# Performance work log

Hardware: AMD Instinct MI355X
Metric: run time of the kernel (lower is better)

Reference implementation:

```python
import jax, jax.numpy as jnp
import numpy as np

B, T, C, H = 2, 64, 384, 768
LR, MOM, DECAY = 0.01, 0.9, 0.001


def pscan(gates, tokens):
    """parallel_scan_log: x[t] = gates[t]*x[t-1] + tokens[t] along axis 1.
    gates [B,S], tokens [B,S,...]."""
    extra = tokens.ndim - gates.ndim
    g = gates.reshape(gates.shape + (1,) * extra)
    g = jnp.clip(g, 1e-7, 1.0 - 1e-7)
    lc = jnp.cumsum(jnp.log(g), axis=1)              # log cumulative gates
    return jnp.exp(lc) * jnp.cumsum(tokens * jnp.exp(-lc), axis=1)


def setup_inputs():
    key = jax.random.key(0)
    ks = jax.random.split(key, 12)
    s = 0.02
    W0 = jax.random.normal(ks[0], (H, C), jnp.float32) * s
    W1 = jax.random.normal(ks[1], (C, H), jnp.float32) * s
    return {
        "x": jax.random.normal(ks[2], (B, T, C), jnp.float32),
        "Wq": jax.random.normal(ks[3], (C, C), jnp.float32) * s, "bq": jnp.zeros((C,), jnp.float32),
        "Wk": jax.random.normal(ks[4], (C, C), jnp.float32) * s, "bk": jnp.zeros((C,), jnp.float32),
        "Wv": jax.random.normal(ks[5], (C, C), jnp.float32) * s, "bv": jnp.zeros((C,), jnp.float32),
        "Wo": jax.random.normal(ks[6], (C, C), jnp.float32) * s, "bo": jnp.zeros((C,), jnp.float32),
        "init_query": jax.random.normal(ks[7], (1, 1, C), jnp.float32) * s,
        "sW0": jnp.broadcast_to(W0, (B, H, C)) + 0.0,
        "sb0": jnp.zeros((B, H), jnp.float32),
        "sW1": jnp.broadcast_to(W1, (B, C, H)) + 0.0,
        "sb1": jnp.zeros((B, C), jnp.float32),
    }


def reference(x, Wq, bq, Wk, bk, Wv, bv, Wo, bo, init_query, sW0, sb0, sW1, sb1):
    dt = x.dtype
    # ---- retrieval (causal: uses init_query since no previous segment) ----
    q = jnp.broadcast_to(init_query, (B, 1, C)) @ Wq.T + bq          # [B,1,C]
    h_pre = jnp.einsum('bqc,bhc->bqh', q, sW0) + sb0[:, None]
    h = h_pre * jax.nn.sigmoid(h_pre)                                 # SiLU
    pred = jnp.einsum('bqh,bch->bqc', h, sW1) + sb1[:, None]
    out = pred @ Wo.T + bo                                            # [B,1,C]

    # ---- test-time memory update: per-token MSE gradients ----
    k = x @ Wk.T + bk                                                 # [B,T,C]
    v = x @ Wv.T + bv
    h1_pre = jnp.einsum('btc,bhc->bth', k, sW0) + sb0[:, None]
    sig = jax.nn.sigmoid(h1_pre)
    h1 = h1_pre * sig
    p = jnp.einsum('bth,bch->btc', h1, sW1) + sb1[:, None]
    dp = p - v                                                        # d(MSE)/d(pred)
    dW1 = jnp.einsum('btc,bth->btch', dp, h1)                         # [B,T,C,H]
    db1 = dp
    dh1 = jnp.einsum('btc,bch->bth', dp, sW1)
    dh1p = dh1 * (sig * (1 + h1_pre * (1 - sig)))                     # SiLU grad
    dW0 = jnp.einsum('bth,btc->bthc', dh1p, k)                        # [B,T,H,C]
    db0 = dh1p

    # ---- momentum scan + decayed weight scan ----
    def update(W, g):
        surprise = -LR * g                                            # [B,T,...]
        m = pscan(jnp.full((B, T), MOM, dt), (1.0 - MOM) * surprise)  # EMA of surprises
        toks = jnp.concatenate([W[:, None], m], axis=1)               # seed with current weight
        gts = jnp.concatenate([jnp.ones((B, 1), dt),
                               jnp.full((B, T), 1.0 - DECAY, dt)], axis=1)
        return pscan(gts, toks)[:, -1]                                # final weight after segment

    nW0 = update(sW0, dW0)
    nb0 = update(sb0, db0)
    nW1 = update(sW1, dW1)
    nb1 = update(sb1, db1)
    return out, nW0, nb0, nW1, nb1
```

## Files before the change

### kernel.cpp

```cpp
#include <hip/hip_runtime.h>
#include <hip/hip_bf16.h>
#include <cmath>

#define BB 2
#define TT 64
#define CC 384
#define HH 768

#define O_OUT 0
#define O_NW0 768
#define O_NB0 (768 + 589824)
#define O_NW1 (O_NB0 + 1536)
#define O_NB1 (O_NW1 + 589824)

struct Coefs { float ct[TT]; float dfac; };

typedef __attribute__((ext_vector_type(8))) short bf16x8;
typedef __attribute__((ext_vector_type(4))) float f32x4;

__device__ __forceinline__ float bf2f(unsigned short u) {
    union { unsigned int i; float f; } x; x.i = ((unsigned int)u) << 16; return x.f;
}
__device__ __forceinline__ unsigned short f2bf(float f) {
    union { float f; unsigned int i; } u; u.f = f;
    unsigned int x = u.i;
    unsigned int r = (x + 0x7fffu + ((x >> 16) & 1u)) >> 16;
    return (unsigned short)r;
}
__device__ __forceinline__ f32x4 mfma16(bf16x8 a, bf16x8 b, f32x4 c) {
    return __builtin_amdgcn_mfma_f32_16x16x32_bf16(a, b, c, 0, 0, 0);
}
__device__ __forceinline__ bf16x8 ldbf8(const unsigned short* p) {
    return *(const bf16x8*)p;
}
__device__ __forceinline__ bf16x8 ldcvt8(const float* p) {
    float4 a = *(const float4*)p, b = *(const float4*)(p + 4);
    bf16x8 r;
    r[0] = (short)f2bf(a.x); r[1] = (short)f2bf(a.y); r[2] = (short)f2bf(a.z); r[3] = (short)f2bf(a.w);
    r[4] = (short)f2bf(b.x); r[5] = (short)f2bf(b.y); r[6] = (short)f2bf(b.z); r[7] = (short)f2bf(b.w);
    return r;
}

__global__ void __launch_bounds__(256) k_qkv(
        const float* __restrict__ x,
        const float* __restrict__ Wk, const float* __restrict__ bk,
        const float* __restrict__ Wv, const float* __restrict__ bv,
        const float* __restrict__ Wq, const float* __restrict__ bq,
        const float* __restrict__ iq,
        const float* __restrict__ sW0, const float* __restrict__ sW1,
        const float* __restrict__ Wo,
        unsigned short* __restrict__ kb_bf, float* __restrict__ vb,
        float* __restrict__ qb, float* __restrict__ warm_sink) {
    const int blk = blockIdx.x, j = threadIdx.x;
    if (blk >= 51) {
        int t = (blk - 51) * 256 + j;
        float acc = 0.f;
        for (int g = t; g < 184320; g += 512 * 256) {
            const float4* src; int off;
            if      (g < 73728)  { src = (const float4*)sW0; off = g; }
            else if (g < 147456) { src = (const float4*)sW1; off = g - 73728; }
            else                 { src = (const float4*)Wo;  off = g - 147456; }
            float4 v = src[off];
            acc += v.x + v.y + v.z + v.w;
        }
        if (acc != acc) warm_sink[0] = acc;
        return;
    }
    const int wid = j >> 6, L = j & 63;
    const int w = blk * 4 + wid;
    const int lrow = L & 15, kq = (L >> 4) * 8, quad = L >> 4;
    int mf, npair;
    if (w < 192) { mf = w % 8; npair = w / 8; }
    else         { mf = 8;     npair = 24 + (w - 192); }
    const float* Arow = (mf < 8) ? (x + (size_t)(mf * 16 + lrow) * CC) : iq;
    const int n0 = npair * 32 + lrow, n1 = n0 + 16;
    const float* B0 = (n0 < CC) ? (Wk + (size_t)n0 * CC)
                    : (n0 < 2 * CC) ? (Wv + (size_t)(n0 - CC) * CC)
                    : (Wq + (size_t)(n0 - 2 * CC) * CC);
    const float* B1 = (n1 < CC) ? (Wk + (size_t)n1 * CC)
                    : (n1 < 2 * CC) ? (Wv + (size_t)(n1 - CC) * CC)
                    : (Wq + (size_t)(n1 - 2 * CC) * CC);
    f32x4 acc0 = {0,0,0,0}, acc1 = {0,0,0,0};
    #pragma unroll 2
    for (int s = 0; s < CC / 32; ++s) {
        int k = s * 32 + kq;
        bf16x8 a = ldcvt8(Arow + k);
        bf16x8 b0 = ldcvt8(B0 + k), b1 = ldcvt8(B1 + k);
        acc0 = mfma16(a, b0, acc0); acc1 = mfma16(a, b1, acc1);
    }
    #pragma unroll
    for (int ni = 0; ni < 2; ++ni) {
        f32x4 acc = ni == 0 ? acc0 : acc1;
        int n = npair * 32 + ni * 16 + lrow;
        if (mf < 8) {
            #pragma unroll
            for (int r = 0; r < 4; ++r) {
                int m = mf * 16 + quad * 4 + r;
                float v = acc[r];
                if (n < CC) kb_bf[(size_t)m * CC + n] = f2bf(v + bk[n]);
                else        vb[(size_t)m * CC + (n - CC)] = v + bv[n - CC];
            }
        } else if (quad == 0) {
            qb[n - 2 * CC] = acc[0] + bq[n - 2 * CC];
        }
    }
}

__global__ void __launch_bounds__(256) k_h1(
        const unsigned short* __restrict__ kb_bf, const float* __restrict__ qb,
        const float* __restrict__ sW0, const float* __restrict__ sb0,
        unsigned short* __restrict__ h1_bf, float* __restrict__ dsil,
        float* __restrict__ hret) {
    const int blk = blockIdx.x, j = threadIdx.x;
    const int b = blk / 30;
    const int wid = j >> 6, L = j & 63;
    const int w = (blk % 30) * 4 + wid;
    const int mf = w % 5, npair = w / 5;
    const int lrow = L & 15, kq = (L >> 4) * 8, quad = L >> 4;
    const unsigned short* Abf = kb_bf + (size_t)(b * TT + mf * 16 + lrow) * CC;
    const int n0 = npair * 32 + lrow;
    const float* B0 = sW0 + (size_t)(b * HH + n0) * CC;
    const float* B1 = B0 + 16 * CC;
    f32x4 acc0 = {0,0,0,0}, acc1 = {0,0,0,0};
    if (mf < 4) {
        #pragma unroll 2
        for (int s = 0; s < CC / 32; ++s) {
            int k = s * 32 + kq;
            bf16x8 a = ldbf8(Abf + k);
            bf16x8 b0 = ldcvt8(B0 + k), b1 = ldcvt8(B1 + k);
            acc0 = mfma16(a, b0, acc0); acc1 = mfma16(a, b1, acc1);
        }
    } else {
        #pragma unroll 2
        for (int s = 0; s < CC / 32; ++s) {
            int k = s * 32 + kq;
            bf16x8 a = ldcvt8(qb + k);
            bf16x8 b0 = ldcvt8(B0 + k), b1 = ldcvt8(B1 + k);
            acc0 = mfma16(a, b0, acc0); acc1 = mfma16(a, b1, acc1);
        }
    }
    #pragma unroll
    for (int ni = 0; ni < 2; ++ni) {
        f32x4 acc = ni == 0 ? acc0 : acc1;
        int n = npair * 32 + ni * 16 + lrow;
        float bias = sb0[b * HH + n];
        if (mf < 4) {
            #pragma unroll
            for (int r = 0; r < 4; ++r) {
                int t = mf * 16 + quad * 4 + r;
                float pre = acc[r] + bias;
                float sig = 1.f / (1.f + expf(-pre));
                size_t idx = (size_t)(b * TT + t) * HH + n;
                h1_bf[idx] = f2bf(pre * sig);
                dsil[idx]  = sig * (1.f + pre * (1.f - sig));
            }
        } else if (quad == 0) {
            float pre = acc[0] + bias;
            float sig = 1.f / (1.f + expf(-pre));
            hret[b * HH + n] = pre * sig;
        }
    }
}

__global__ void __launch_bounds__(256) k_p(
        const unsigned short* __restrict__ h1_bf, const float* __restrict__ hret,
        const float* __restrict__ vb,
        const float* __restrict__ sW1, const float* __restrict__ sb1,
        unsigned short* __restrict__ dp_bf, float* __restrict__ pred) {
    const int blk = blockIdx.x, j = threadIdx.x;
    const int b = blk / 15;
    const int wid = j >> 6, L = j & 63;
    const int w = (blk % 15) * 4 + wid;
    const int mf = w % 5, npair = w / 5;
    const int lrow = L & 15, kq = (L >> 4) * 8, quad = L >> 4;
    const unsigned short* Abf = h1_bf + (size_t)(b * TT + mf * 16 + lrow) * HH;
    const float* Aq = hret + (size_t)b * HH;
    const int n0 = npair * 32 + lrow;
    const float* B0 = sW1 + (size_t)(b * CC + n0) * HH;
    const float* B1 = B0 + 16 * HH;
    f32x4 acc0 = {0,0,0,0}, acc1 = {0,0,0,0};
    if (mf < 4) {
        #pragma unroll 2
        for (int s = 0; s < HH / 32; ++s) {
            int k = s * 32 + kq;
            bf16x8 a = ldbf8(Abf + k);
            bf16x8 b0 = ldcvt8(B0 + k), b1 = ldcvt8(B1 + k);
            acc0 = mfma16(a, b0, acc0); acc1 = mfma16(a, b1, acc1);
        }
    } else {
        #pragma unroll 2
        for (int s = 0; s < HH / 32; ++s) {
            int k = s * 32 + kq;
            bf16x8 a = ldcvt8(Aq + k);
            bf16x8 b0 = ldcvt8(B0 + k), b1 = ldcvt8(B1 + k);
            acc0 = mfma16(a, b0, acc0); acc1 = mfma16(a, b1, acc1);
        }
    }
    #pragma unroll
    for (int ni = 0; ni < 2; ++ni) {
        f32x4 acc = ni == 0 ? acc0 : acc1;
        int n = npair * 32 + ni * 16 + lrow;
        float bias = sb1[b * CC + n];
        if (mf < 4) {
            #pragma unroll
            for (int r = 0; r < 4; ++r) {
                int t = mf * 16 + quad * 4 + r;
                size_t idx = (size_t)(b * TT + t) * CC + n;
                dp_bf[idx] = f2bf(acc[r] + bias - vb[idx]);
            }
        } else if (quad == 0) {
            pred[b * CC + n] = acc[0] + bias;
        }
    }
}

__global__ void __launch_bounds__(256) k_epi(
        const unsigned short* __restrict__ dp_bf,
        const unsigned short* __restrict__ h1_bf,
        const unsigned short* __restrict__ kb_bf,
        const float* __restrict__ dsil,
        const float* __restrict__ sW0, const float* __restrict__ sb0,
        const float* __restrict__ sW1, const float* __restrict__ sb1,
        const float* __restrict__ pred,
        const float* __restrict__ Wo, const float* __restrict__ bo,
        float* __restrict__ out, Coefs cf) {
    __shared__ __align__(16) unsigned char sbuf[49920];
    const int blk = blockIdx.x, j = threadIdx.x;
    if (blk < 288) {
        float* a_t = (float*)sbuf;
        float* e_t = (float*)(sbuf + 8192);
        const int b = blk / 144, rem = blk % 144;
        const int c0 = (rem / 12) * 32, h0 = (rem % 12) * 64;
        for (int i = j; i < TT * 32; i += 256) {
            int t = i >> 5, c = i & 31;
            a_t[t * 32 + c] = cf.ct[t] * bf2f(dp_bf[((size_t)(b * TT + t)) * CC + c0 + c]);
        }
        for (int i = j; i < TT * 64; i += 256) {
            int t = i >> 6, h = i & 63;
            e_t[t * 64 + h] = bf2f(h1_bf[((size_t)(b * TT + t)) * HH + h0 + h]);
        }
        __syncthreads();
        const int ci = j & 31, hb = (j >> 5) * 8;
        float acc[8] = {0, 0, 0, 0, 0, 0, 0, 0};
        for (int t = 0; t < TT; ++t) {
            float av = a_t[t * 32 + ci];
            #pragma unroll
            for (int m = 0; m < 8; ++m) acc[m] += av * e_t[t * 64 + hb + m];
        }
        const size_t idx = ((size_t)b * CC + c0 + ci) * HH + h0 + hb;
        const float4* w4 = (const float4*)(sW1 + idx);
        float4 wa = w4[0], wb = w4[1];
        float4 o0, o1;
        o0.x = cf.dfac * wa.x - acc[0]; o0.y = cf.dfac * wa.y - acc[1];
        o0.z = cf.dfac * wa.z - acc[2]; o0.w = cf.dfac * wa.w - acc[3];
        o1.x = cf.dfac * wb.x - acc[4]; o1.y = cf.dfac * wb.y - acc[5];
        o1.z = cf.dfac * wb.z - acc[6]; o1.w = cf.dfac * wb.w - acc[7];
        *(float4*)(out + O_NW1 + idx) = o0;
        *(float4*)(out + O_NW1 + idx + 4) = o1;
        if (h0 == 0 && j < 32) {
            float s = 0.f;
            for (int t = 0; t < TT; ++t) s += a_t[t * 32 + j];
            out[O_NB1 + b * CC + c0 + j] = cf.dfac * sb1[b * CC + c0 + j] - s;
        }
    } else if (blk < 576) {
        unsigned short* ldsT = (unsigned short*)sbuf;
        float* a_t = (float*)(sbuf + 25344);
        float* e_t = (float*)(sbuf + 25344 + 8192);
        const int u = blk - 288;
        const int b = u / 144, rem = u % 144;
        const int h0 = (rem / 6) * 32, c0 = (rem % 6) * 64;
        {
            const int hl = j & 31, cs = j >> 5;
            const float* base = sW1 + (size_t)b * CC * HH + h0 + hl;
            for (int c = cs; c < CC; c += 8)
                ldsT[c * 33 + hl] = f2bf(base[(size_t)c * HH]);
        }
        for (int i = j; i < TT * 64; i += 256) {
            int t = i >> 6, c = i & 63;
            e_t[t * 64 + c] = bf2f(kb_bf[((size_t)(b * TT + t)) * CC + c0 + c]);
        }
        __syncthreads();
        const int wid = j >> 6, L = j & 63;
        const int lrow = L & 15, kq = (L >> 4) * 8, quad = L >> 4;
        const unsigned short* Abf = dp_bf + (size_t)(b * TT + wid * 16 + lrow) * CC;
        f32x4 acc0 = {0,0,0,0}, acc1 = {0,0,0,0};
        for (int s = 0; s < CC / 32; ++s) {
            int k = s * 32 + kq;
            bf16x8 a = ldbf8(Abf + k);
            bf16x8 b0, b1;
            #pragma unroll
            for (int i = 0; i < 8; ++i) {
                b0[i] = (short)ldsT[(k + i) * 33 + lrow];
                b1[i] = (short)ldsT[(k + i) * 33 + 16 + lrow];
            }
            acc0 = mfma16(a, b0, acc0); acc1 = mfma16(a, b1, acc1);
        }
        #pragma unroll
        for (int ni = 0; ni < 2; ++ni) {
            f32x4 acc = ni == 0 ? acc0 : acc1;
            int hl = ni * 16 + lrow;
            #pragma unroll
            for (int r = 0; r < 4; ++r) {
                int t = wid * 16 + quad * 4 + r;
                float ds = dsil[(size_t)(b * TT + t) * HH + h0 + hl];
                a_t[t * 32 + hl] = cf.ct[t] * (acc[r] * ds);
            }
        }
        __syncthreads();
        const int hi = j & 31, cb = (j >> 5) * 8;
        float acc[8] = {0, 0, 0, 0, 0, 0, 0, 0};
        for (int t = 0; t < TT; ++t) {
            float av = a_t[t * 32 + hi];
            #pragma unroll
            for (int m = 0; m < 8; ++m) acc[m] += av * e_t[t * 64 + cb + m];
        }
        const size_t idx = ((size_t)b * HH + h0 + hi) * CC + c0 + cb;
        const float4* w4 = (const float4*)(sW0 + idx);
        float4 wa = w4[0], wb = w4[1];
        float4 o0, o1;
        o0.x = cf.dfac * wa.x - acc[0]; o0.y = cf.dfac * wa.y - acc[1];
        o0.z = cf.dfac * wa.z - acc[2]; o0.w = cf.dfac * wa.w - acc[3];
        o1.x = cf.dfac * wb.x - acc[4]; o1.y = cf.dfac * wb.y - acc[5];
        o1.z = cf.dfac * wb.z - acc[6]; o1.w = cf.dfac * wb.w - acc[7];
        *(float4*)(out + O_NW0 + idx) = o0;
        *(float4*)(out + O_NW0 + idx + 4) = o1;
        if (c0 == 0 && j < 32) {
            float s = 0.f;
            for (int t = 0; t < TT; ++t) s += a_t[t * 32 + j];
            out[O_NB0 + b * HH + h0 + j] = cf.dfac * sb0[b * HH + h0 + j] - s;
        }
    } else {
        float* vecs = (float*)sbuf;
        float* part = (float*)(sbuf + 4096);
        const int rb = blk - 576;
        const int b = rb / 24, nt = rb % 24;
        if (j < CC / 4) ((float4*)vecs)[j] = ((const float4*)(pred + b * CC))[j];
        __syncthreads();
        const int nl = j & 15, ks = j >> 4;
        const int n = nt * 16 + nl;
        const float4* wr = (const float4*)(Wo + (size_t)n * CC + ks * 24);
        float s = 0.f;
        #pragma unroll
        for (int i = 0; i < 6; ++i) {
            float4 a = wr[i];
            const float* v = vecs + ks * 24 + i * 4;
            s += a.x * v[0] + a.y * v[1] + a.z * v[2] + a.w * v[3];
        }
        part[ks * 17 + nl] = s;
        __syncthreads();
        if (j < 16) {
            int n2 = nt * 16 + j;
            float acc = bo[n2];
            #pragma unroll
            for (int kk = 0; kk < 16; ++kk) acc += part[kk * 17 + j];
            out[O_OUT + b * CC + n2] = acc;
        }
    }
}

extern "C" void kernel_launch(void* const* d_in, const int* in_sizes, int n_in,
                              void* d_out, int out_size, void* d_ws, size_t ws_size,
                              hipStream_t stream) {
    const float* x   = (const float*)d_in[0];
    const float* Wq  = (const float*)d_in[1];
    const float* bq  = (const float*)d_in[2];
    const float* Wk  = (const float*)d_in[3];
    const float* bk  = (const float*)d_in[4];
    const float* Wv  = (const float*)d_in[5];
    const float* bv  = (const float*)d_in[6];
    const float* Wo  = (const float*)d_in[7];
    const float* bo  = (const float*)d_in[8];
    const float* iq  = (const float*)d_in[9];
    const float* sW0 = (const float*)d_in[10];
    const float* sb0 = (const float*)d_in[11];
    const float* sW1 = (const float*)d_in[12];
    const float* sb1 = (const float*)d_in[13];

    float* fw = (float*)d_ws;
    float* qb   = fw;
    float* hret = qb + 384;
    float* pred = hret + 1536;
    float* vb   = pred + 768;
    float* dsil = vb + 49152;
    float* warm = dsil + 98304;
    unsigned short* us = (unsigned short*)(warm + 4);
    unsigned short* kb_bf = us;
    unsigned short* h1_bf = kb_bf + 49152;
    unsigned short* dp_bf = h1_bf + 98304;

    Coefs cf;
    const double mom = 0.9, decay = 1.0 - 0.001, lr = 0.01;
    for (int s = 0; s < TT; ++s) {
        double sum = 0.0;
        for (int t = s; t < TT; ++t) sum += pow(decay, (double)(TT - 1 - t)) * pow(mom, (double)(t - s));
        cf.ct[s] = (float)(lr * (1.0 - mom) * sum);
    }
    cf.dfac = (float)pow(decay, (double)TT);

    k_qkv<<<dim3(563), dim3(256), 0, stream>>>(x, Wk, bk, Wv, bv, Wq, bq, iq, sW0, sW1, Wo,
                                               kb_bf, vb, qb, warm);
    k_h1 <<<dim3(60),  dim3(256), 0, stream>>>(kb_bf, qb, sW0, sb0, h1_bf, dsil, hret);
    k_p  <<<dim3(30),  dim3(256), 0, stream>>>(h1_bf, hret, vb, sW1, sb1, dp_bf, pred);
    k_epi<<<dim3(624), dim3(256), 0, stream>>>(dp_bf, h1_bf, kb_bf, dsil, sW0, sb0, sW1, sb1,
                                               pred, Wo, bo, (float*)d_out, cf);
}
```

Baseline: 137.0 us.

## Fuse four kernels into one persistent kernel with grid-wide barriers

Merges the qkv, h1, p and epilogue kernels into a single persistent launch of 312 blocks. Stages are separated by atomic-counter grid barriers, and the epilogue's 624 tiles are looped over the resident blocks. The aim is to remove per-kernel launch overhead and inter-kernel gaps. In exchange it adds a memset, spin-wait barriers, and idle blocks during the small middle stages, and it depends on every block being co-resident.

```diff
diff --git a/kernel.cpp b/kernel.cpp
--- a/kernel.cpp
+++ b/kernel.cpp
@@ -12,6 +12,8 @@
 #define O_NB0 (768 + 589824)
 #define O_NW1 (O_NB0 + 1536)
 #define O_NB1 (O_NW1 + 589824)
+
+#define GRID_BLKS 312
 
 struct Coefs { float ct[TT]; float dfac; };
 
@@ -41,319 +43,320 @@
     return r;
 }
 
-__global__ void __launch_bounds__(256) k_qkv(
-        const float* __restrict__ x,
-        const float* __restrict__ Wk, const float* __restrict__ bk,
-        const float* __restrict__ Wv, const float* __restrict__ bv,
-        const float* __restrict__ Wq, const float* __restrict__ bq,
-        const float* __restrict__ iq,
-        const float* __restrict__ sW0, const float* __restrict__ sW1,
-        const float* __restrict__ Wo,
-        unsigned short* __restrict__ kb_bf, float* __restrict__ vb,
-        float* __restrict__ qb, float* __restrict__ warm_sink) {
+struct KArgs {
+    const float *x, *Wq, *bq, *Wk, *bk, *Wv, *bv, *Wo, *bo, *iq;
+    const float *sW0, *sb0, *sW1, *sb1;
+    unsigned short *kb_bf, *h1_bf, *dp_bf;
+    float *vb, *qb, *hret, *pred, *dsil, *warm;
+    unsigned *bar;
+    float *out;
+    Coefs cf;
+};
+
+__device__ __forceinline__ void gsync(unsigned* bar, int which) {
+    __syncthreads();
+    if (threadIdx.x == 0) {
+        unsigned* c = bar + which * 32;
+        __threadfence();
+        __hip_atomic_fetch_add(c, 1u, __ATOMIC_ACQ_REL, __HIP_MEMORY_SCOPE_AGENT);
+        while (__hip_atomic_load(c, __ATOMIC_ACQUIRE, __HIP_MEMORY_SCOPE_AGENT) < GRID_BLKS)
+            __builtin_amdgcn_s_sleep(2);
+    }
+    __syncthreads();
+}
+
+__global__ void __launch_bounds__(256, 2) fused(KArgs A) {
+    __shared__ __align__(16) unsigned char sbuf[49920];
     const int blk = blockIdx.x, j = threadIdx.x;
-    if (blk >= 51) {
-        int t = (blk - 51) * 256 + j;
-        float acc = 0.f;
-        for (int g = t; g < 184320; g += 512 * 256) {
-            const float4* src; int off;
-            if      (g < 73728)  { src = (const float4*)sW0; off = g; }
-            else if (g < 147456) { src = (const float4*)sW1; off = g - 73728; }
-            else                 { src = (const float4*)Wo;  off = g - 147456; }
-            float4 v = src[off];
-            acc += v.x + v.y + v.z + v.w;
-        }
-        if (acc != acc) warm_sink[0] = acc;
-        return;
-    }
-    const int wid = j >> 6, L = j & 63;
-    const int w = blk * 4 + wid;
-    const int lrow = L & 15, kq = (L >> 4) * 8, quad = L >> 4;
-    int mf, npair;
-    if (w < 192) { mf = w % 8; npair = w / 8; }
-    else         { mf = 8;     npair = 24 + (w - 192); }
-    const float* Arow = (mf < 8) ? (x + (size_t)(mf * 16 + lrow) * CC) : iq;
-    const int n0 = npair * 32 + lrow, n1 = n0 + 16;
-    const float* B0 = (n0 < CC) ? (Wk + (size_t)n0 * CC)
-                    : (n0 < 2 * CC) ? (Wv + (size_t)(n0 - CC) * CC)
-                    : (Wq + (size_t)(n0 - 2 * CC) * CC);
-    const float* B1 = (n1 < CC) ? (Wk + (size_t)n1 * CC)
-                    : (n1 < 2 * CC) ? (Wv + (size_t)(n1 - CC) * CC)
-                    : (Wq + (size_t)(n1 - 2 * CC) * CC);
-    f32x4 acc0 = {0,0,0,0}, acc1 = {0,0,0,0};
-    #pragma unroll 2
-    for (int s = 0; s < CC / 32; ++s) {
-        int k = s * 32 + kq;
-        bf16x8 a = ldcvt8(Arow + k);
-        bf16x8 b0 = ldcvt8(B0 + k), b1 = ldcvt8(B1 + k);
-        acc0 = mfma16(a, b0, acc0); acc1 = mfma16(a, b1, acc1);
-    }
-    #pragma unroll
-    for (int ni = 0; ni < 2; ++ni) {
-        f32x4 acc = ni == 0 ? acc0 : acc1;
-        int n = npair * 32 + ni * 16 + lrow;
-        if (mf < 8) {
-            #pragma unroll
-            for (int r = 0; r < 4; ++r) {
-                int m = mf * 16 + quad * 4 + r;
-                float v = acc[r];
-                if (n < CC) kb_bf[(size_t)m * CC + n] = f2bf(v + bk[n]);
-                else        vb[(size_t)m * CC + (n - CC)] = v + bv[n - CC];
-            }
-        } else if (quad == 0) {
-            qb[n - 2 * CC] = acc[0] + bq[n - 2 * CC];
-        }
-    }
-}
-
-__global__ void __launch_bounds__(256) k_h1(
-        const unsigned short* __restrict__ kb_bf, const float* __restrict__ qb,
-        const float* __restrict__ sW0, const float* __restrict__ sb0,
-        unsigned short* __restrict__ h1_bf, float* __restrict__ dsil,
-        float* __restrict__ hret) {
-    const int blk = blockIdx.x, j = threadIdx.x;
-    const int b = blk / 30;
-    const int wid = j >> 6, L = j & 63;
-    const int w = (blk % 30) * 4 + wid;
-    const int mf = w % 5, npair = w / 5;
-    const int lrow = L & 15, kq = (L >> 4) * 8, quad = L >> 4;
-    const unsigned short* Abf = kb_bf + (size_t)(b * TT + mf * 16 + lrow) * CC;
-    const int n0 = npair * 32 + lrow;
-    const float* B0 = sW0 + (size_t)(b * HH + n0) * CC;
-    const float* B1 = B0 + 16 * CC;
-    f32x4 acc0 = {0,0,0,0}, acc1 = {0,0,0,0};
-    if (mf < 4) {
+
+    if (blk < 51) {
+        const int wid = j >> 6, L = j & 63;
+        const int w = blk * 4 + wid;
+        const int lrow = L & 15, kq = (L >> 4) * 8, quad = L >> 4;
+        int mf, npair;
+        if (w < 192) { mf = w % 8; npair = w / 8; }
+        else         { mf = 8;     npair = 24 + (w - 192); }
+        const float* Arow = (mf < 8) ? (A.x + (size_t)(mf * 16 + lrow) * CC) : A.iq;
+        const int n0 = npair * 32 + lrow, n1 = n0 + 16;
+        const float* B0 = (n0 < CC) ? (A.Wk + (size_t)n0 * CC)
+                        : (n0 < 2 * CC) ? (A.Wv + (size_t)(n0 - CC) * CC)
+                        : (A.Wq + (size_t)(n0 - 2 * CC) * CC);
+        const float* B1 = (n1 < CC) ? (A.Wk + (size_t)n1 * CC)
+                        : (n1 < 2 * CC) ? (A.Wv + (size_t)(n1 - CC) * CC)
+                        : (A.Wq + (size_t)(n1 - 2 * CC) * CC);
+        f32x4 acc0 = {0,0,0,0}, acc1 = {0,0,0,0};
         #pragma unroll 2
         for (int s = 0; s < CC / 32; ++s) {
             int k = s * 32 + kq;
-            bf16x8 a = ldbf8(Abf + k);
+            bf16x8 a = ldcvt8(Arow + k);
             bf16x8 b0 = ldcvt8(B0 + k), b1 = ldcvt8(B1 + k);
-            acc0 = mfma16(a, b0, acc0); acc1 = mfma16(a, b1, acc1);
-        }
-    } else {
-        #pragma unroll 2
-        for (int s = 0; s < CC / 32; ++s) {
-            int k = s * 32 + kq;
-            bf16x8 a = ldcvt8(qb + k);
-            bf16x8 b0 = ldcvt8(B0 + k), b1 = ldcvt8(B1 + k);
-            acc0 = mfma16(a, b0, acc0); acc1 = mfma16(a, b1, acc1);
-        }
-    }
-    #pragma unroll
-    for (int ni = 0; ni < 2; ++ni) {
-        f32x4 acc = ni == 0 ? acc0 : acc1;
-        int n = npair * 32 + ni * 16 + lrow;
-        float bias = sb0[b * HH + n];
-        if (mf < 4) {
-            #pragma unroll
-            for (int r = 0; r < 4; ++r) {
-                int t = mf * 16 + quad * 4 + r;
-                float pre = acc[r] + bias;
-                float sig = 1.f / (1.f + expf(-pre));
-                size_t idx = (size_t)(b * TT + t) * HH + n;
-                h1_bf[idx] = f2bf(pre * sig);
-                dsil[idx]  = sig * (1.f + pre * (1.f - sig));
-            }
-        } else if (quad == 0) {
-            float pre = acc[0] + bias;
-            float sig = 1.f / (1.f + expf(-pre));
-            hret[b * HH + n] = pre * sig;
-        }
-    }
-}
-
-__global__ void __launch_bounds__(256) k_p(
-        const unsigned short* __restrict__ h1_bf, const float* __restrict__ hret,
-        const float* __restrict__ vb,
-        const float* __restrict__ sW1, const float* __restrict__ sb1,
-        unsigned short* __restrict__ dp_bf, float* __restrict__ pred) {
-    const int blk = blockIdx.x, j = threadIdx.x;
-    const int b = blk / 15;
-    const int wid = j >> 6, L = j & 63;
-    const int w = (blk % 15) * 4 + wid;
-    const int mf = w % 5, npair = w / 5;
-    const int lrow = L & 15, kq = (L >> 4) * 8, quad = L >> 4;
-    const unsigned short* Abf = h1_bf + (size_t)(b * TT + mf * 16 + lrow) * HH;
-    const float* Aq = hret + (size_t)b * HH;
-    const int n0 = npair * 32 + lrow;
-    const float* B0 = sW1 + (size_t)(b * CC + n0) * HH;
-    const float* B1 = B0 + 16 * HH;
-    f32x4 acc0 = {0,0,0,0}, acc1 = {0,0,0,0};
-    if (mf < 4) {
-        #pragma unroll 2
-        for (int s = 0; s < HH / 32; ++s) {
-            int k = s * 32 + kq;
-            bf16x8 a = ldbf8(Abf + k);
-            bf16x8 b0 = ldcvt8(B0 + k), b1 = ldcvt8(B1 + k);
-            acc0 = mfma16(a, b0, acc0); acc1 = mfma16(a, b1, acc1);
-        }
-    } else {
-        #pragma unroll 2
-        for (int s = 0; s < HH / 32; ++s) {
-            int k = s * 32 + kq;
-            bf16x8 a = ldcvt8(Aq + k);
-            bf16x8 b0 = ldcvt8(B0 + k), b1 = ldcvt8(B1 + k);
-            acc0 = mfma16(a, b0, acc0); acc1 = mfma16(a, b1, acc1);
-        }
-    }
-    #pragma unroll
-    for (int ni = 0; ni < 2; ++ni) {
-        f32x4 acc = ni == 0 ? acc0 : acc1;
-        int n = npair * 32 + ni * 16 + lrow;
-        float bias = sb1[b * CC + n];
-        if (mf < 4) {
-            #pragma unroll
-            for (int r = 0; r < 4; ++r) {
-                int t = mf * 16 + quad * 4 + r;
-                size_t idx = (size_t)(b * TT + t) * CC + n;
-                dp_bf[idx] = f2bf(acc[r] + bias - vb[idx]);
-            }
-        } else if (quad == 0) {
-            pred[b * CC + n] = acc[0] + bias;
-        }
-    }
-}
-
-__global__ void __launch_bounds__(256) k_epi(
-        const unsigned short* __restrict__ dp_bf,
-        const unsigned short* __restrict__ h1_bf,
-        const unsigned short* __restrict__ kb_bf,
-        const float* __restrict__ dsil,
-        const float* __restrict__ sW0, const float* __restrict__ sb0,
-        const float* __restrict__ sW1, const float* __restrict__ sb1,
-        const float* __restrict__ pred,
-        const float* __restrict__ Wo, const float* __restrict__ bo,
-        float* __restrict__ out, Coefs cf) {
-    __shared__ __align__(16) unsigned char sbuf[49920];
-    const int blk = blockIdx.x, j = threadIdx.x;
-    if (blk < 288) {
-        float* a_t = (float*)sbuf;
-        float* e_t = (float*)(sbuf + 8192);
-        const int b = blk / 144, rem = blk % 144;
-        const int c0 = (rem / 12) * 32, h0 = (rem % 12) * 64;
-        for (int i = j; i < TT * 32; i += 256) {
-            int t = i >> 5, c = i & 31;
-            a_t[t * 32 + c] = cf.ct[t] * bf2f(dp_bf[((size_t)(b * TT + t)) * CC + c0 + c]);
-        }
-        for (int i = j; i < TT * 64; i += 256) {
-            int t = i >> 6, h = i & 63;
-            e_t[t * 64 + h] = bf2f(h1_bf[((size_t)(b * TT + t)) * HH + h0 + h]);
-        }
-        __syncthreads();
-        const int ci = j & 31, hb = (j >> 5) * 8;
-        float acc[8] = {0, 0, 0, 0, 0, 0, 0, 0};
-        for (int t = 0; t < TT; ++t) {
-            float av = a_t[t * 32 + ci];
-            #pragma unroll
-            for (int m = 0; m < 8; ++m) acc[m] += av * e_t[t * 64 + hb + m];
-        }
-        const size_t idx = ((size_t)b * CC + c0 + ci) * HH + h0 + hb;
-        const float4* w4 = (const float4*)(sW1 + idx);
-        float4 wa = w4[0], wb = w4[1];
-        float4 o0, o1;
-        o0.x = cf.dfac * wa.x - acc[0]; o0.y = cf.dfac * wa.y - acc[1];
-        o0.z = cf.dfac * wa.z - acc[2]; o0.w = cf.dfac * wa.w - acc[3];
-        o1.x = cf.dfac * wb.x - acc[4]; o1.y = cf.dfac * wb.y - acc[5];
-        o1.z = cf.dfac * wb.z - acc[6]; o1.w = cf.dfac * wb.w - acc[7];
-        *(float4*)(out + O_NW1 + idx) = o0;
-        *(float4*)(out + O_NW1 + idx + 4) = o1;
-        if (h0 == 0 && j < 32) {
-            float s = 0.f;
-            for (int t = 0; t < TT; ++t) s += a_t[t * 32 + j];
-            out[O_NB1 + b * CC + c0 + j] = cf.dfac * sb1[b * CC + c0 + j] - s;
-        }
-    } else if (blk < 576) {
-        unsigned short* ldsT = (unsigned short*)sbuf;
-        float* a_t = (float*)(sbuf + 25344);
-        float* e_t = (float*)(sbuf + 25344 + 8192);
-        const int u = blk - 288;
-        const int b = u / 144, rem = u % 144;
-        const int h0 = (rem / 6) * 32, c0 = (rem % 6) * 64;
-        {
-            const int hl = j & 31, cs = j >> 5;
-            const float* base = sW1 + (size_t)b * CC * HH + h0 + hl;
-            for (int c = cs; c < CC; c += 8)
-                ldsT[c * 33 + hl] = f2bf(base[(size_t)c * HH]);
-        }
-        for (int i = j; i < TT * 64; i += 256) {
-            int t = i >> 6, c = i & 63;
-            e_t[t * 64 + c] = bf2f(kb_bf[((size_t)(b * TT + t)) * CC + c0 + c]);
-        }
-        __syncthreads();
-        const int wid = j >> 6, L = j & 63;
-        const int lrow = L & 15, kq = (L >> 4) * 8, quad = L >> 4;
-        const unsigned short* Abf = dp_bf + (size_t)(b * TT + wid * 16 + lrow) * CC;
-        f32x4 acc0 = {0,0,0,0}, acc1 = {0,0,0,0};
-        for (int s = 0; s < CC / 32; ++s) {
-            int k = s * 32 + kq;
-            bf16x8 a = ldbf8(Abf + k);
-            bf16x8 b0, b1;
-            #pragma unroll
-            for (int i = 0; i < 8; ++i) {
-                b0[i] = (short)ldsT[(k + i) * 33 + lrow];
-                b1[i] = (short)ldsT[(k + i) * 33 + 16 + lrow];
-            }
             acc0 = mfma16(a, b0, acc0); acc1 = mfma16(a, b1, acc1);
         }
         #pragma unroll
         for (int ni = 0; ni < 2; ++ni) {
             f32x4 acc = ni == 0 ? acc0 : acc1;
-            int hl = ni * 16 + lrow;
+            int n = npair * 32 + ni * 16 + lrow;
+            if (mf < 8) {
+                #pragma unroll
+                for (int r = 0; r < 4; ++r) {
+                    int m = mf * 16 + quad * 4 + r;
+                    float v = acc[r];
+                    if (n < CC) A.kb_bf[(size_t)m * CC + n] = f2bf(v + A.bk[n]);
+                    else        A.vb[(size_t)m * CC + (n - CC)] = v + A.bv[n - CC];
+                }
+            } else if (quad == 0) {
+                A.qb[n - 2 * CC] = acc[0] + A.bq[n - 2 * CC];
+            }
+        }
+    } else {
+        int t = (blk - 51) * 256 + j;
+        float acc = 0.f;
+        for (int g = t; g < 331776; g += (GRID_BLKS - 51) * 256) {
+            const float4* src; int off;
+            if      (g < 147456) { src = (const float4*)A.sW0; off = g; }
+            else if (g < 294912) { src = (const float4*)A.sW1; off = g - 147456; }
+            else                 { src = (const float4*)A.Wo;  off = g - 294912; }
+            float4 v = src[off];
+            acc += v.x + v.y + v.z + v.w;
+        }
+        if (acc != acc) A.warm[0] = acc;
+    }
+
+    gsync(A.bar, 0);
+
+    if (blk < 60) {
+        const int b = blk / 30;
+        const int wid = j >> 6, L = j & 63;
+        const int w = (blk % 30) * 4 + wid;
+        const int mf = w % 5, npair = w / 5;
+        const int lrow = L & 15, kq = (L >> 4) * 8, quad = L >> 4;
+        const unsigned short* Abf = A.kb_bf + (size_t)(b * TT + mf * 16 + lrow) * CC;
+        const int n0 = npair * 32 + lrow;
+        const float* B0 = A.sW0 + (size_t)(b * HH + n0) * CC;
+        const float* B1 = B0 + 16 * CC;
+        f32x4 acc0 = {0,0,0,0}, acc1 = {0,0,0,0};
+        if (mf < 4) {
+            #pragma unroll 2
+            for (int s = 0; s < CC / 32; ++s) {
+                int k = s * 32 + kq;
+                bf16x8 a = ldbf8(Abf + k);
+                bf16x8 b0 = ldcvt8(B0 + k), b1 = ldcvt8(B1 + k);
+                acc0 = mfma16(a, b0, acc0); acc1 = mfma16(a, b1, acc1);
+            }
+        } else {
+            #pragma unroll 2
+            for (int s = 0; s < CC / 32; ++s) {
+                int k = s * 32 + kq;
+                bf16x8 a = ldcvt8(A.qb + k);
+                bf16x8 b0 = ldcvt8(B0 + k), b1 = ldcvt8(B1 + k);
+                acc0 = mfma16(a, b0, acc0); acc1 = mfma16(a, b1, acc1);
+            }
+        }
+        #pragma unroll
+        for (int ni = 0; ni < 2; ++ni) {
+            f32x4 acc = ni == 0 ? acc0 : acc1;
+            int n = npair * 32 + ni * 16 + lrow;
+            float bias = A.sb0[b * HH + n];
+            if (mf < 4) {
+                #pragma unroll
+                for (int r = 0; r < 4; ++r) {
+                    int t = mf * 16 + quad * 4 + r;
+                    float pre = acc[r] + bias;
+                    float sig = 1.f / (1.f + expf(-pre));
+                    size_t idx = (size_t)(b * TT + t) * HH + n;
+                    A.h1_bf[idx] = f2bf(pre * sig);
+                    A.dsil[idx]  = sig * (1.f + pre * (1.f - sig));
+                }
+            } else if (quad == 0) {
+                float pre = acc[0] + bias;
+                float sig = 1.f / (1.f + expf(-pre));
+                A.hret[b * HH + n] = pre * sig;
+            }
+        }
+    }
+
+    gsync(A.bar, 1);
+
+    if (blk < 30) {
+        const int b = blk / 15;
+        const int wid = j >> 6, L = j & 63;
+        const int w = (blk % 15) * 4 + wid;
+        const int mf = w % 5, npair = w / 5;
+        const int lrow = L & 15, kq = (L >> 4) * 8, quad = L >> 4;
+        const unsigned short* Abf = A.h1_bf + (size_t)(b * TT + mf * 16 + lrow) * HH;
+        const float* Aq = A.hret + (size_t)b * HH;
+        const int n0 = npair * 32 + lrow;
+        const float* B0 = A.sW1 + (size_t)(b * CC + n0) * HH;
+        const float* B1 = B0 + 16 * HH;
+        f32x4 acc0 = {0,0,0,0}, acc1 = {0,0,0,0};
+        if (mf < 4) {
+            #pragma unroll 2
+            for (int s = 0; s < HH / 32; ++s) {
+                int k = s * 32 + kq;
+                bf16x8 a = ldbf8(Abf + k);
+                bf16x8 b0 = ldcvt8(B0 + k), b1 = ldcvt8(B1 + k);
+                acc0 = mfma16(a, b0, acc0); acc1 = mfma16(a, b1, acc1);
+            }
+        } else {
+            #pragma unroll 2
+            for (int s = 0; s < HH / 32; ++s) {
+                int k = s * 32 + kq;
+                bf16x8 a = ldcvt8(Aq + k);
+                bf16x8 b0 = ldcvt8(B0 + k), b1 = ldcvt8(B1 + k);
+                acc0 = mfma16(a, b0, acc0); acc1 = mfma16(a, b1, acc1);
+            }
+        }
+        #pragma unroll
+        for (int ni = 0; ni < 2; ++ni) {
+            f32x4 acc = ni == 0 ? acc0 : acc1;
+            int n = npair * 32 + ni * 16 + lrow;
+            float bias = A.sb1[b * CC + n];
+            if (mf < 4) {
+                #pragma unroll
+                for (int r = 0; r < 4; ++r) {
+                    int t = mf * 16 + quad * 4 + r;
+                    size_t idx = (size_t)(b * TT + t) * CC + n;
+                    A.dp_bf[idx] = f2bf(acc[r] + bias - A.vb[idx]);
+                }
+            } else if (quad == 0) {
+                A.pred[b * CC + n] = acc[0] + bias;
+            }
+        }
+    }
+
+    gsync(A.bar, 2);
+
+    for (int tile = blk; tile < 624; tile += GRID_BLKS) {
+        __syncthreads();
+        if (tile < 288) {
+            float* a_t = (float*)sbuf;
+            float* e_t = (float*)(sbuf + 8192);
+            const int b = tile / 144, rem = tile % 144;
+            const int c0 = (rem / 12) * 32, h0 = (rem % 12) * 64;
+            for (int i = j; i < TT * 32; i += 256) {
+                int t = i >> 5, c = i & 31;
+                a_t[t * 32 + c] = A.cf.ct[t] * bf2f(A.dp_bf[((size_t)(b * TT + t)) * CC + c0 + c]);
+            }
+            for (int i = j; i < TT * 64; i += 256) {
+                int t = i >> 6, h = i & 63;
+                e_t[t * 64 + h] = bf2f(A.h1_bf[((size_t)(b * TT + t)) * HH + h0 + h]);
+            }
+            __syncthreads();
+            const int ci = j & 31, hb = (j >> 5) * 8;
+            float acc[8] = {0, 0, 0, 0, 0, 0, 0, 0};
+            for (int t = 0; t < TT; ++t) {
+                float av = a_t[t * 32 + ci];
+                #pragma unroll
+                for (int m = 0; m < 8; ++m) acc[m] += av * e_t[t * 64 + hb + m];
+            }
+            const size_t idx = ((size_t)b * CC + c0 + ci) * HH + h0 + hb;
+            const float4* w4 = (const float4*)(A.sW1 + idx);
+            float4 wa = w4[0], wb = w4[1];
+            float4 o0, o1;
+            o0.x = A.cf.dfac * wa.x - acc[0]; o0.y = A.cf.dfac * wa.y - acc[1];
+            o0.z = A.cf.dfac * wa.z - acc[2]; o0.w = A.cf.dfac * wa.w - acc[3];
+            o1.x = A.cf.dfac * wb.x - acc[4]; o1.y = A.cf.dfac * wb.y - acc[5];
+            o1.z = A.cf.dfac * wb.z - acc[6]; o1.w = A.cf.dfac * wb.w - acc[7];
+            *(float4*)(A.out + O_NW1 + idx) = o0;
+            *(float4*)(A.out + O_NW1 + idx + 4) = o1;
+            if (h0 == 0 && j < 32) {
+                float s = 0.f;
+                for (int t = 0; t < TT; ++t) s += a_t[t * 32 + j];
+                A.out[O_NB1 + b * CC + c0 + j] = A.cf.dfac * A.sb1[b * CC + c0 + j] - s;
+            }
+        } else if (tile < 576) {
+            unsigned short* ldsT = (unsigned short*)sbuf;
+            float* a_t = (float*)(sbuf + 25344);
+            float* e_t = (float*)(sbuf + 25344 + 8192);
+            const int u = tile - 288;
+            const int b = u / 144, rem = u % 144;
+            const int h0 = (rem / 6) * 32, c0 = (rem % 6) * 64;
+            {
+                const int hl = j & 31, cs = j >> 5;
+                const float* base = A.sW1 + (size_t)b * CC * HH + h0 + hl;
+                for (int c = cs; c < CC; c += 8)
+                    ldsT[c * 33 + hl] = f2bf(base[(size_t)c * HH]);
+            }
+            for (int i = j; i < TT * 64; i += 256) {
+                int t = i >> 6, c = i & 63;
+                e_t[t * 64 + c] = bf2f(A.kb_bf[((size_t)(b * TT + t)) * CC + c0 + c]);
+            }
+            __syncthreads();
+            const int wid = j >> 6, L = j & 63;
+            const int lrow = L & 15, kq = (L >> 4) * 8, quad = L >> 4;
+            const unsigned short* Abf = A.dp_bf + (size_t)(b * TT + wid * 16 + lrow) * CC;
+            f32x4 acc0 = {0,0,0,0}, acc1 = {0,0,0,0};
+            for (int s = 0; s < CC / 32; ++s) {
+                int k = s * 32 + kq;
+                bf16x8 a = ldbf8(Abf + k);
+                bf16x8 b0, b1;
+                #pragma unroll
+                for (int i = 0; i < 8; ++i) {
+                    b0[i] = (short)ldsT[(k + i) * 33 + lrow];
+                    b1[i] = (short)ldsT[(k + i) * 33 + 16 + lrow];
+                }
+                acc0 = mfma16(a, b0, acc0); acc1 = mfma16(a, b1, acc1);
+            }
             #pragma unroll
-            for (int r = 0; r < 4; ++r) {
-                int t = wid * 16 + quad * 4 + r;
-                float ds = dsil[(size_t)(b * TT + t) * HH + h0 + hl];
-                a_t[t * 32 + hl] = cf.ct[t] * (acc[r] * ds);
-            }
-        }
-        __syncthreads();
-        const int hi = j & 31, cb = (j >> 5) * 8;
-        float acc[8] = {0, 0, 0, 0, 0, 0, 0, 0};
-        for (int t = 0; t < TT; ++t) {
-            float av = a_t[t * 32 + hi];
+            for (int ni = 0; ni < 2; ++ni) {
+                f32x4 acc = ni == 0 ? acc0 : acc1;
+                int hl = ni * 16 + lrow;
+                #pragma unroll
+                for (int r = 0; r < 4; ++r) {
+                    int t = wid * 16 + quad * 4 + r;
+                    float ds = A.dsil[(size_t)(b * TT + t) * HH + h0 + hl];
+                    a_t[t * 32 + hl] = A.cf.ct[t] * (acc[r] * ds);
+                }
+            }
+            __syncthreads();
+            const int hi = j & 31, cb = (j >> 5) * 8;
+            float acc[8] = {0, 0, 0, 0, 0, 0, 0, 0};
+            for (int t = 0; t < TT; ++t) {
+                float av = a_t[t * 32 + hi];
+                #pragma unroll
+                for (int m = 0; m < 8; ++m) acc[m] += av * e_t[t * 64 + cb + m];
+            }
+            const size_t idx = ((size_t)b * HH + h0 + hi) * CC + c0 + cb;
+            const float4* w4 = (const float4*)(A.sW0 + idx);
+            float4 wa = w4[0], wb = w4[1];
+            float4 o0, o1;
+            o0.x = A.cf.dfac * wa.x - acc[0]; o0.y = A.cf.dfac * wa.y - acc[1];
+            o0.z = A.cf.dfac * wa.z - acc[2]; o0.w = A.cf.dfac * wa.w - acc[3];
+            o1.x = A.cf.dfac * wb.x - acc[4]; o1.y = A.cf.dfac * wb.y - acc[5];
+            o1.z = A.cf.dfac * wb.z - acc[6]; o1.w = A.cf.dfac * wb.w - acc[7];
+            *(float4*)(A.out + O_NW0 + idx) = o0;
+            *(float4*)(A.out + O_NW0 + idx + 4) = o1;
+            if (c0 == 0 && j < 32) {
+                float s = 0.f;
+                for (int t = 0; t < TT; ++t) s += a_t[t * 32 + j];
+                A.out[O_NB0 + b * HH + h0 + j] = A.cf.dfac * A.sb0[b * HH + h0 + j] - s;
+            }
+        } else {
+            float* vecs = (float*)sbuf;
+            float* part = (float*)(sbuf + 4096);
+            const int rb = tile - 576;
+            const int b = rb / 24, nt = rb % 24;
+            if (j < CC / 4) ((float4*)vecs)[j] = ((const float4*)(A.pred + b * CC))[j];
+            __syncthreads();
+            const int nl = j & 15, ks = j >> 4;
+            const int n = nt * 16 + nl;
+            const float4* wr = (const float4*)(A.Wo + (size_t)n * CC + ks * 24);
+            float s = 0.f;
             #pragma unroll
-            for (int m = 0; m < 8; ++m) acc[m] += av * e_t[t * 64 + cb + m];
-        }
-        const size_t idx = ((size_t)b * HH + h0 + hi) * CC + c0 + cb;
-        const float4* w4 = (const float4*)(sW0 + idx);
-        float4 wa = w4[0], wb = w4[1];
-        float4 o0, o1;
-        o0.x = cf.dfac * wa.x - acc[0]; o0.y = cf.dfac * wa.y - acc[1];
-        o0.z = cf.dfac * wa.z - acc[2]; o0.w = cf.dfac * wa.w - acc[3];
-        o1.x = cf.dfac * wb.x - acc[4]; o1.y = cf.dfac * wb.y - acc[5];
-        o1.z = cf.dfac * wb.z - acc[6]; o1.w = cf.dfac * wb.w - acc[7];
-        *(float4*)(out + O_NW0 + idx) = o0;
-        *(float4*)(out + O_NW0 + idx + 4) = o1;
-        if (c0 == 0 && j < 32) {
-            float s = 0.f;
-            for (int t = 0; t < TT; ++t) s += a_t[t * 32 + j];
-            out[O_NB0 + b * HH + h0 + j] = cf.dfac * sb0[b * HH + h0 + j] - s;
-        }
-    } else {
-        float* vecs = (float*)sbuf;
-        float* part = (float*)(sbuf + 4096);
-        const int rb = blk - 576;
-        const int b = rb / 24, nt = rb % 24;
-        if (j < CC / 4) ((float4*)vecs)[j] = ((const float4*)(pred + b * CC))[j];
-        __syncthreads();
-        const int nl = j & 15, ks = j >> 4;
-        const int n = nt * 16 + nl;
-        const float4* wr = (const float4*)(Wo + (size_t)n * CC + ks * 24);
-        float s = 0.f;
-        #pragma unroll
-        for (int i = 0; i < 6; ++i) {
-            float4 a = wr[i];
-            const float* v = vecs + ks * 24 + i * 4;
-            s += a.x * v[0] + a.y * v[1] + a.z * v[2] + a.w * v[3];
-        }
-        part[ks * 17 + nl] = s;
-        __syncthreads();
-        if (j < 16) {
-            int n2 = nt * 16 + j;
-            float acc = bo[n2];
-            #pragma unroll
-            for (int kk = 0; kk < 16; ++kk) acc += part[kk * 17 + j];
-            out[O_OUT + b * CC + n2] = acc;
+            for (int i = 0; i < 6; ++i) {
+                float4 a4 = wr[i];
+                const float* v = vecs + ks * 24 + i * 4;
+                s += a4.x * v[0] + a4.y * v[1] + a4.z * v[2] + a4.w * v[3];
+            }
+            part[ks * 17 + nl] = s;
+            __syncthreads();
+            if (j < 16) {
+                int n2 = nt * 16 + j;
+                float acc = A.bo[n2];
+                #pragma unroll
+                for (int kk = 0; kk < 16; ++kk) acc += part[kk * 17 + j];
+                A.out[O_OUT + b * CC + n2] = acc;
+            }
         }
     }
 }
@@ -361,46 +364,45 @@
 extern "C" void kernel_launch(void* const* d_in, const int* in_sizes, int n_in,
                               void* d_out, int out_size, void* d_ws, size_t ws_size,
                               hipStream_t stream) {
-    const float* x   = (const float*)d_in[0];
-    const float* Wq  = (const float*)d_in[1];
-    const float* bq  = (const float*)d_in[2];
-    const float* Wk  = (const float*)d_in[3];
-    const float* bk  = (const float*)d_in[4];
-    const float* Wv  = (const float*)d_in[5];
-    const float* bv  = (const float*)d_in[6];
-    const float* Wo  = (const float*)d_in[7];
-    const float* bo  = (const float*)d_in[8];
-    const float* iq  = (const float*)d_in[9];
-    const float* sW0 = (const float*)d_in[10];
-    const float* sb0 = (const float*)d_in[11];
-    const float* sW1 = (const float*)d_in[12];
-    const float* sb1 = (const float*)d_in[13];
-
-    float* fw = (float*)d_ws;
-    float* qb   = fw;
-    float* hret = qb + 384;
-    float* pred = hret + 1536;
-    float* vb   = pred + 768;
-    float* dsil = vb + 49152;
-    float* warm = dsil + 98304;
-    unsigned short* us = (unsigned short*)(warm + 4);
-    unsigned short* kb_bf = us;
-    unsigned short* h1_bf = kb_bf + 49152;
-    unsigned short* dp_bf = h1_bf + 98304;
-
-    Coefs cf;
+    KArgs a;
+    a.x   = (const float*)d_in[0];
+    a.Wq  = (const float*)d_in[1];
+    a.bq  = (const float*)d_in[2];
+    a.Wk  = (const float*)d_in[3];
+    a.bk  = (const float*)d_in[4];
+    a.Wv  = (const float*)d_in[5];
+    a.bv  = (const float*)d_in[6];
+    a.Wo  = (const float*)d_in[7];
+    a.bo  = (const float*)d_in[8];
+    a.iq  = (const float*)d_in[9];
+    a.sW0 = (const float*)d_in[10];
+    a.sb0 = (const float*)d_in[11];
+    a.sW1 = (const float*)d_in[12];
+    a.sb1 = (const float*)d_in[13];
+
+    a.bar  = (unsigned*)d_ws;
+    float* fw = (float*)d_ws + 128;
+    a.qb   = fw;
+    a.hret = a.qb + 384;
+    a.pred = a.hret + 1536;
+    a.vb   = a.pred + 768;
+    a.dsil = a.vb + 49152;
+    a.warm = a.dsil + 98304;
+    unsigned short* us = (unsigned short*)(a.warm + 4);
+    a.kb_bf = us;
+    a.h1_bf = a.kb_bf + 49152;
+    a.dp_bf = a.h1_bf + 98304;
+
+    a.out = (float*)d_out;
+
     const double mom = 0.9, decay = 1.0 - 0.001, lr = 0.01;
     for (int s = 0; s < TT; ++s) {
         double sum = 0.0;
         for (int t = s; t < TT; ++t) sum += pow(decay, (double)(TT - 1 - t)) * pow(mom, (double)(t - s));
-        cf.ct[s] = (float)(lr * (1.0 - mom) * sum);
-    }
-    cf.dfac = (float)pow(decay, (double)TT);
-
-    k_qkv<<<dim3(563), dim3(256), 0, stream>>>(x, Wk, bk, Wv, bv, Wq, bq, iq, sW0, sW1, Wo,
-                                               kb_bf, vb, qb, warm);
-    k_h1 <<<dim3(60),  dim3(256), 0, stream>>>(kb_bf, qb, sW0, sb0, h1_bf, dsil, hret);
-    k_p  <<<dim3(30),  dim3(256), 0, stream>>>(h1_bf, hret, vb, sW1, sb1, dp_bf, pred);
-    k_epi<<<dim3(624), dim3(256), 0, stream>>>(dp_bf, h1_bf, kb_bf, dsil, sW0, sb0, sW1, sb1,
-                                               pred, Wo, bo, (float*)d_out, cf);
-}
+        a.cf.ct[s] = (float)(lr * (1.0 - mom) * sum);
+    }
+    a.cf.dfac = (float)pow(decay, (double)TT);
+
+    hipMemsetAsync(a.bar, 0, 512, stream);
+    fused<<<dim3(GRID_BLKS), dim3(256), 0, stream>>>(a);
+}
```

New measurement: 284.9 us. 108% more time.
